# Kernel tuning notes

Hardware: AMD Instinct MI355X
Metric: run time of the kernel (lower is better)

## Reference

```python
import jax, jax.numpy as jnp
import numpy as np
from math import factorial

L_MAX = 3
K = 256
N = 2048


def _cg_coeff(l1, m1, l2, m2, l3, m3):
    # Clebsch-Gordan coefficient <l1 m1 l2 m2 | l3 m3> via the Racah formula.
    if m3 != m1 + m2:
        return 0.0
    pref = ((2 * l3 + 1) * factorial(l3 + l1 - l2) * factorial(l3 - l1 + l2)
            * factorial(l1 + l2 - l3) / factorial(l1 + l2 + l3 + 1)) ** 0.5
    pref *= (factorial(l3 + m3) * factorial(l3 - m3) * factorial(l1 - m1)
             * factorial(l1 + m1) * factorial(l2 - m2) * factorial(l2 + m2)) ** 0.5
    s = 0.0
    for k in range(0, l1 + l2 - l3 + 1):
        d = [k, l1 + l2 - l3 - k, l1 - m1 - k, l2 + m2 - k,
             l3 - l2 + m1 + k, l3 - l1 - m2 + k]
        if min(d) < 0:
            continue
        den = 1.0
        for x in d:
            den *= factorial(x)
        s += (-1.0) ** k / den
    return pref * s


def _cg_tensor(l1, l2, l3):
    out = np.zeros((2 * l1 + 1, 2 * l2 + 1, 2 * l3 + 1), dtype=np.float32)
    for m1 in range(-l1, l1 + 1):
        for m2 in range(-l2, l2 + 1):
            m3 = m1 + m2
            if -l3 <= m3 <= l3:
                out[m1 + l1, m2 + l2, m3 + l3] = _cg_coeff(l1, m1, l2, m2, l3, m3)
    return jnp.asarray(out)


# All (l1, l2) -> l coupling paths allowed by the triangle inequality, l <= L_MAX.
PATHS = {l: [(l1, l2) for l1 in range(L_MAX + 1) for l2 in range(L_MAX + 1)
             if abs(l1 - l2) <= l <= l1 + l2] for l in range(L_MAX + 1)}
CG = {(l1, l2, l): _cg_tensor(l1, l2, l)
      for l in range(L_MAX + 1) for (l1, l2) in PATHS[l]}


def _forward(f1, f2, U, W):
    outs = []
    for l in range(L_MAX + 1):
        # CG tensor product: elementwise over channels k, coupled over (m1, m2) -> m.
        parts = [jnp.einsum('abm,nak,nbk->nmk', CG[(l1, l2, l)], f1[l1], f2[l2])
                 for (l1, l2) in PATHS[l]]
        tp = jnp.concatenate(parts, axis=-1)          # [N, 2l+1, n_paths(l)*K]
        mixed = jnp.einsum('nmc,ck->nmk', tp, U[l])   # U_dict per-l mixing -> [N, 2l+1, K]
        mixed = jnp.einsum('nmk,kj->nmj', mixed, W[l])  # learned per-l linear
        outs.append(f1[l] + mixed)                    # residual
    return tuple(outs)


def setup_inputs() -> dict:
    key = jax.random.key(0)
    ks = jax.random.split(key, 16)
    inp = {}
    for l in range(L_MAX + 1):
        inp[f'f1_l{l}'] = jax.random.normal(ks[l], (N, 2 * l + 1, K), jnp.float32)
        inp[f'f2_l{l}'] = jax.random.normal(ks[4 + l], (N, 2 * l + 1, K), jnp.float32)
        cin = len(PATHS[l]) * K
        inp[f'U_{l}'] = jax.random.normal(ks[8 + l], (cin, K), jnp.float32) / float(np.sqrt(cin))
        inp[f'W_{l}'] = jax.random.normal(ks[12 + l], (K, K), jnp.float32) / float(np.sqrt(K))
    return inp


def reference(f1_l0, f1_l1, f1_l2, f1_l3,
              f2_l0, f2_l1, f2_l2, f2_l3,
              U_0, U_1, U_2, U_3,
              W_0, W_1, W_2, W_3):
    f1 = [f1_l0, f1_l1, f1_l2, f1_l3]
    f2 = [f2_l0, f2_l1, f2_l2, f2_l3]
    U = [U_0, U_1, U_2, U_3]
    W = [W_0, W_1, W_2, W_3]
    return _forward(f1, f2, U, W)
```

## Files before the change

kernel.cpp:

```cpp
#include <hip/hip_runtime.h>
#include <math.h>

typedef __attribute__((ext_vector_type(4))) float f32x4;
typedef __attribute__((ext_vector_type(8))) __bf16 bf16x8;
typedef __attribute__((ext_vector_type(4))) __bf16 bf16x4;

__device__ __constant__ int GP_L[34]  = {0,0,0,0, 1,1,1,1,1,1,1,1,1, 2,2,2,2,2,2,2,2,2,2,2, 3,3,3,3,3,3,3,3,3,3};
__device__ __constant__ int GP_L1[34] = {0,1,2,3, 0,1,1,1,2,2,2,3,3, 0,1,1,1,2,2,2,2,3,3,3, 0,1,1,2,2,2,3,3,3,3};
__device__ __constant__ int GP_L2[34] = {0,1,2,3, 1,0,1,2,1,2,3,2,3, 2,1,2,3,0,1,2,3,1,2,3, 3,2,3,1,2,3,0,1,2,3};

__device__ double dfact(int n) { double r = 1.0; for (int i = 2; i <= n; ++i) r *= (double)i; return r; }

__device__ double cg_coeff(int l1, int m1, int l2, int m2, int l3, int m3) {
  if (m3 != m1 + m2) return 0.0;
  double pref = sqrt((2.0 * l3 + 1.0) * dfact(l3 + l1 - l2) * dfact(l3 - l1 + l2)
                     * dfact(l1 + l2 - l3) / dfact(l1 + l2 + l3 + 1));
  pref *= sqrt(dfact(l3 + m3) * dfact(l3 - m3) * dfact(l1 - m1) * dfact(l1 + m1)
               * dfact(l2 - m2) * dfact(l2 + m2));
  double s = 0.0;
  for (int k = 0; k <= l1 + l2 - l3; ++k) {
    int d0 = k, d1 = l1 + l2 - l3 - k, d2 = l1 - m1 - k, d3 = l2 + m2 - k;
    int d4 = l3 - l2 + m1 + k, d5 = l3 - l1 - m2 + k;
    if (d0 < 0 || d1 < 0 || d2 < 0 || d3 < 0 || d4 < 0 || d5 < 0) continue;
    double den = dfact(d0) * dfact(d1) * dfact(d2) * dfact(d3) * dfact(d4) * dfact(d5);
    s += ((k & 1) ? -1.0 : 1.0) / den;
  }
  return pref * s;
}

__global__ void cg_init(float* __restrict__ cg) {
  int idx = blockIdx.x * 256 + threadIdx.x;
  if (idx >= 34 * 49) return;
  int gp = idx / 49, r = idx % 49;
  int m1i = r / 7, m2i = r % 7;
  int l3 = GP_L[gp], l1 = GP_L1[gp], l2 = GP_L2[gp];
  float v = 0.f;
  if (m1i <= 2 * l1 && m2i <= 2 * l2) {
    int m1 = m1i - l1, m2 = m2i - l2, m3 = m1 + m2;
    if (m3 >= -l3 && m3 <= l3) v = (float)cg_coeff(l1, m1, l2, m2, l3, m3);
  }
  cg[idx] = v;
}

__global__ __launch_bounds__(256) void cvt_u_all(
    const float* __restrict__ u0, const float* __restrict__ u1,
    const float* __restrict__ u2, const float* __restrict__ u3,
    __bf16* __restrict__ out) {
  long i = (long)blockIdx.x * 256 + threadIdx.x;
  const long b1 = 65536, b2 = 212992, b3 = 393216;
  const float* src; long s;
  if (i < b1)      { src = u0; s = i; }
  else if (i < b2) { src = u1; s = i - b1; }
  else if (i < b3) { src = u2; s = i - b2; }
  else             { src = u3; s = i - b3; }
  float4 v = ((const float4*)src)[s];
  bf16x4 o;
  o[0] = (__bf16)v.x; o[1] = (__bf16)v.y; o[2] = (__bf16)v.z; o[3] = (__bf16)v.w;
  ((bf16x4*)out)[i] = o;
}

__global__ void wt_cvt_all(const float* __restrict__ w0, const float* __restrict__ w1,
                           const float* __restrict__ w2, const float* __restrict__ w3,
                           __bf16* __restrict__ Wt) {
  int b = blockIdx.x;
  int l = b >> 8, j = b & 255, k = threadIdx.x;
  const float* W = (l == 0) ? w0 : (l == 1) ? w1 : (l == 2) ? w2 : w3;
  Wt[((long)l << 16) + (j << 8) + k] = (__bf16)W[(k << 8) + j];
}

template <int l1, int l2, int L>
__device__ __forceinline__ void tp_path2(const float* __restrict__ v1, const float* __restrict__ v2,
                                         const float* __restrict__ cgt, float* __restrict__ tp) {
#pragma unroll
  for (int a = 0; a < 2 * l1 + 1; ++a) {
#pragma unroll
    for (int b = 0; b < 2 * l2 + 1; ++b) {
      int mi = a + b - l1 - l2 + L;
      if (mi >= 0 && mi <= 2 * L)
        tp[mi] = fmaf(cgt[a * 7 + b], v1[a] * v2[b], tp[mi]);
    }
  }
}

#define TPW(LV, DST, CIN, GOFF, P, L1V, L2V)                                    \
  { float tp[2 * (LV) + 1] = {};                                                \
    tp_path2<L1V, L2V, LV>(v1 + CUM[L1V], v2 + CUM[L2V], cg + ((GOFF) + (P)) * 49, tp); \
    __bf16* o = (DST) + (n * (2 * (LV) + 1)) * (CIN) + (P) * 256 + k;           \
    _Pragma("unroll")                                                           \
    for (int m = 0; m < 2 * (LV) + 1; ++m) o[(long)m * (CIN)] = (__bf16)tp[m]; }

template <int LMASK>
__global__ __launch_bounds__(256) void tp_all(
    const float* __restrict__ f10, const float* __restrict__ f11,
    const float* __restrict__ f12, const float* __restrict__ f13,
    const float* __restrict__ f20, const float* __restrict__ f21,
    const float* __restrict__ f22, const float* __restrict__ f23,
    const float* __restrict__ cg,
    __bf16* __restrict__ A0, __bf16* __restrict__ A1,
    __bf16* __restrict__ A2, __bf16* __restrict__ A3) {
  const long n = blockIdx.x;
  const int k = threadIdx.x;
  constexpr int CUM[4] = {0, 1, 4, 9};
  const float* f1s[4] = {f10, f11, f12, f13};
  const float* f2s[4] = {f20, f21, f22, f23};

  float v1[16], v2[16];
#pragma unroll
  for (int l1 = 0; l1 < 4; ++l1) {
    const float* p1 = f1s[l1] + (n * (2 * l1 + 1)) * 256 + k;
    const float* p2 = f2s[l1] + (n * (2 * l1 + 1)) * 256 + k;
#pragma unroll
    for (int a = 0; a < 2 * l1 + 1; ++a) {
      v1[CUM[l1] + a] = p1[(long)a * 256];
      v2[CUM[l1] + a] = p2[(long)a * 256];
    }
  }

  if constexpr (LMASK & 1) {
    TPW(0, A0, 1024, 0, 0, 0, 0)  TPW(0, A0, 1024, 0, 1, 1, 1)
    TPW(0, A0, 1024, 0, 2, 2, 2)  TPW(0, A0, 1024, 0, 3, 3, 3)
  }
  if constexpr (LMASK & 2) {
    TPW(1, A1, 2304, 4, 0, 0, 1)  TPW(1, A1, 2304, 4, 1, 1, 0)
    TPW(1, A1, 2304, 4, 2, 1, 1)  TPW(1, A1, 2304, 4, 3, 1, 2)
    TPW(1, A1, 2304, 4, 4, 2, 1)  TPW(1, A1, 2304, 4, 5, 2, 2)
    TPW(1, A1, 2304, 4, 6, 2, 3)  TPW(1, A1, 2304, 4, 7, 3, 2)
    TPW(1, A1, 2304, 4, 8, 3, 3)
  }
  if constexpr (LMASK & 4) {
    TPW(2, A2, 2816, 13, 0, 0, 2)  TPW(2, A2, 2816, 13, 1, 1, 1)
    TPW(2, A2, 2816, 13, 2, 1, 2)  TPW(2, A2, 2816, 13, 3, 1, 3)
    TPW(2, A2, 2816, 13, 4, 2, 0)  TPW(2, A2, 2816, 13, 5, 2, 1)
    TPW(2, A2, 2816, 13, 6, 2, 2)  TPW(2, A2, 2816, 13, 7, 2, 3)
    TPW(2, A2, 2816, 13, 8, 3, 1)  TPW(2, A2, 2816, 13, 9, 3, 2)
    TPW(2, A2, 2816, 13, 10, 3, 3)
  }
  if constexpr (LMASK & 8) {
    TPW(3, A3, 2560, 24, 0, 0, 3)  TPW(3, A3, 2560, 24, 1, 1, 2)
    TPW(3, A3, 2560, 24, 2, 1, 3)  TPW(3, A3, 2560, 24, 3, 2, 1)
    TPW(3, A3, 2560, 24, 4, 2, 2)  TPW(3, A3, 2560, 24, 5, 2, 3)
    TPW(3, A3, 2560, 24, 6, 3, 0)  TPW(3, A3, 2560, 24, 7, 3, 1)
    TPW(3, A3, 2560, 24, 8, 3, 2)  TPW(3, A3, 2560, 24, 9, 3, 3)
  }
}

struct GemmDesc {
  const __bf16* A[4];
  const __bf16* B[4];
  void*         C[4];
  const float*  R[4];
  int start[4];
  int lmap[4];
  int Kd[4];
  int Nc[4];
};

__device__ __forceinline__ void gload_lds16(const void* g, void* l) {
  __builtin_amdgcn_global_load_lds((const __attribute__((address_space(1))) void*)g,
                                   (__attribute__((address_space(3))) void*)l, 16, 0, 0);
}

template <bool OUT_BF16, bool RESID>
__global__ __launch_bounds__(256) void gemm_batched(GemmDesc d) {
  __shared__ __bf16 As[128 * 64];
  __shared__ __bf16 Bs[128 * 64];
  const int tid = threadIdx.x;
  const int bid = blockIdx.x;
  int seg = 0;
  if (bid >= d.start[1]) seg = 1;
  if (bid >= d.start[2]) seg = 2;
  if (bid >= d.start[3]) seg = 3;
  const int l = d.lmap[seg];
  const int rel = bid - d.start[seg];
  const int Kd = d.Kd[l], Nc = d.Nc[l];
  const int nTN = Nc >> 7;
  const int tM = rel / nTN, tN = rel % nTN;

  const int lane = tid & 63, wave = tid >> 6;
  const int wm = (wave >> 1) << 6, wn = (wave & 1) << 6;
  const int lr = lane & 15, lk = (lane >> 4) << 3;

  f32x4 acc[4][4] = {};

  const int r32 = tid >> 3;
  const int sl = ((tid & 7) ^ (r32 & 7)) << 3;
  const __bf16* Ag = d.A[l] + (long)(tM * 128 + r32) * Kd + sl;
  const __bf16* Bg = d.B[l] + (long)(tN * 128 + r32) * Kd + sl;
  char* AsB = (char*)As;
  char* BsB = (char*)Bs;

  for (int kt = 0; kt < Kd; kt += 64) {
#pragma unroll
    for (int i = 0; i < 4; ++i) {
      gload_lds16(Ag + (long)i * 32 * Kd + kt, AsB + i * 4096 + tid * 16);
      gload_lds16(Bg + (long)i * 32 * Kd + kt, BsB + i * 4096 + tid * 16);
    }
    __syncthreads();

#pragma unroll
    for (int kk = 0; kk < 64; kk += 32) {
      bf16x8 af[4], bfr[4];
#pragma unroll
      for (int mi = 0; mi < 4; ++mi)
        af[mi] = *(const bf16x8*)(AsB + ((wm + mi * 16 + lr) << 7)
                                      + ((((kk + lk) << 1)) ^ ((lr & 7) << 4)));
#pragma unroll
      for (int ni = 0; ni < 4; ++ni)
        bfr[ni] = *(const bf16x8*)(BsB + ((wn + ni * 16 + lr) << 7)
                                       + ((((kk + lk) << 1)) ^ ((lr & 7) << 4)));
#pragma unroll
      for (int mi = 0; mi < 4; ++mi)
#pragma unroll
        for (int ni = 0; ni < 4; ++ni)
          acc[mi][ni] = __builtin_amdgcn_mfma_f32_16x16x32_bf16(af[mi], bfr[ni], acc[mi][ni], 0, 0, 0);
    }
    __syncthreads();
  }

  const long col0 = (long)tN * 128 + wn + lr;
  const long row0 = (long)tM * 128 + wm + ((lane >> 4) << 2);
#pragma unroll
  for (int mi = 0; mi < 4; ++mi) {
#pragma unroll
    for (int j = 0; j < 4; ++j) {
      long r = row0 + mi * 16 + j;
      long base = r * (long)Nc + col0;
#pragma unroll
      for (int ni = 0; ni < 4; ++ni) {
        long idx = base + ni * 16;
        float v = acc[mi][ni][j];
        if constexpr (RESID) v += d.R[l][idx];
        if constexpr (OUT_BF16) ((__bf16*)d.C[l])[idx] = (__bf16)v;
        else                    ((float*)d.C[l])[idx] = v;
      }
    }
  }
}

extern "C" void kernel_launch(void* const* d_in, const int* in_sizes, int n_in,
                              void* d_out, int out_size, void* d_ws, size_t ws_size,
                              hipStream_t stream) {
  const float* F1[4], * F2[4], * Uin[4], * Win[4];
  for (int l = 0; l < 4; ++l) {
    F1[l]  = (const float*)d_in[4 * l + 0];
    F2[l]  = (const float*)d_in[4 * l + 1];
    Uin[l] = (const float*)d_in[4 * l + 2];
    Win[l] = (const float*)d_in[4 * l + 3];
  }
  static const int  cin_[4]  = {1024, 2304, 2816, 2560};
  static const int  cum_[4]  = {0, 1024, 3328, 6144};
  static const long moff_[4] = {0, 524288, 2097152, 4718592};
  static const int  Ml_[4]   = {2048, 6144, 10240, 14336};
  static const long asz_[4]  = {4194304L, 28311552L, 57671680L, 73400320L};

  char* ws = (char*)d_ws;
  float*  cg   = (float*)ws;
  __bf16* Ubf  = (__bf16*)(ws + 8192);
  __bf16* Wtbf = (__bf16*)(ws + 8192 + 4456448);
  __bf16* UWt  = (__bf16*)(ws + 5242880);
  const long ABASE = 10485760;
  const bool big = ws_size >= (size_t)(ABASE + asz_[0] + asz_[1] + asz_[2] + asz_[3]);

  __bf16* Ab[4];
  if (big) {
    long off = ABASE;
    for (int l = 0; l < 4; ++l) { Ab[l] = (__bf16*)(ws + off); off += asz_[l]; }
  } else {
    for (int l = 0; l < 4; ++l) Ab[l] = (__bf16*)(ws + ABASE);
  }

  hipLaunchKernelGGL(cg_init, dim3(7), dim3(256), 0, stream, cg);
  hipLaunchKernelGGL(cvt_u_all, dim3(2176), dim3(256), 0, stream,
                     Uin[0], Uin[1], Uin[2], Uin[3], Ubf);
  hipLaunchKernelGGL(wt_cvt_all, dim3(1024), dim3(256), 0, stream,
                     Win[0], Win[1], Win[2], Win[3], Wtbf);

  {
    GemmDesc d;
    int starts[4] = {0, 40, 84, 120};
    int lmap[4]   = {3, 2, 1, 0};
    for (int s = 0; s < 4; ++s) { d.start[s] = starts[s]; d.lmap[s] = lmap[s]; }
    for (int l = 0; l < 4; ++l) {
      d.A[l] = Wtbf + (long)l * 65536;
      d.B[l] = Ubf + (long)cum_[l] * 256;
      d.C[l] = (void*)(UWt + (long)cum_[l] * 256);
      d.R[l] = nullptr;
      d.Kd[l] = 256;
      d.Nc[l] = cin_[l];
    }
    hipLaunchKernelGGL((gemm_batched<true, false>), dim3(136), dim3(256), 0, stream, d);
  }

  if (big) {
    hipLaunchKernelGGL((tp_all<15>), dim3(2048), dim3(256), 0, stream,
                       F1[0], F1[1], F1[2], F1[3], F2[0], F2[1], F2[2], F2[3],
                       cg, Ab[0], Ab[1], Ab[2], Ab[3]);
    GemmDesc d;
    int starts[4] = {0, 224, 384, 480};
    int lmap[4]   = {3, 2, 1, 0};
    for (int s = 0; s < 4; ++s) { d.start[s] = starts[s]; d.lmap[s] = lmap[s]; }
    for (int l = 0; l < 4; ++l) {
      d.A[l] = Ab[l];
      d.B[l] = UWt + (long)cum_[l] * 256;
      d.C[l] = (void*)((float*)d_out + moff_[l]);
      d.R[l] = F1[l];
      d.Kd[l] = cin_[l];
      d.Nc[l] = 256;
    }
    hipLaunchKernelGGL((gemm_batched<false, true>), dim3(512), dim3(256), 0, stream, d);
  } else {
    for (int l = 0; l < 4; ++l) {
      switch (l) {
        case 0: hipLaunchKernelGGL((tp_all<1>), dim3(2048), dim3(256), 0, stream,
                  F1[0],F1[1],F1[2],F1[3], F2[0],F2[1],F2[2],F2[3], cg,
                  Ab[0],Ab[1],Ab[2],Ab[3]); break;
        case 1: hipLaunchKernelGGL((tp_all<2>), dim3(2048), dim3(256), 0, stream,
                  F1[0],F1[1],F1[2],F1[3], F2[0],F2[1],F2[2],F2[3], cg,
                  Ab[0],Ab[1],Ab[2],Ab[3]); break;
        case 2: hipLaunchKernelGGL((tp_all<4>), dim3(2048), dim3(256), 0, stream,
                  F1[0],F1[1],F1[2],F1[3], F2[0],F2[1],F2[2],F2[3], cg,
                  Ab[0],Ab[1],Ab[2],Ab[3]); break;
        case 3: hipLaunchKernelGGL((tp_all<8>), dim3(2048), dim3(256), 0, stream,
                  F1[0],F1[1],F1[2],F1[3], F2[0],F2[1],F2[2],F2[3], cg,
                  Ab[0],Ab[1],Ab[2],Ab[3]); break;
      }
      GemmDesc d;
      for (int s = 0; s < 4; ++s) {
        d.start[s] = (s == 0) ? 0 : 0x7fffffff;
        d.lmap[s] = l;
      }
      for (int ll = 0; ll < 4; ++ll) {
        d.A[ll] = Ab[l];
        d.B[ll] = UWt + (long)cum_[l] * 256;
        d.C[ll] = (void*)((float*)d_out + moff_[l]);
        d.R[ll] = F1[l];
        d.Kd[ll] = cin_[l];
        d.Nc[ll] = 256;
      }
      hipLaunchKernelGGL((gemm_batched<false, true>), dim3((Ml_[l] >> 7) * 2), dim3(256),
                         0, stream, d);
    }
  }
  (void)in_sizes; (void)n_in; (void)out_size; (void)ws_size;
}
```

Baseline: 152.6 us.

## Fuse tensor product generation into GEMM, computing A tiles directly in LDS

Replaces the separate tensor-product kernel and the big GEMM with one fused kernel. Each K-tile of the A operand (the CG products) is computed on the fly into swizzled LDS while the UW weight tile streams in via global_load_lds, and MFMA accumulation follows with the residual added at the end. This removes the write and re-read of the large bf16 intermediate A buffers (up to roughly 160MB) and one launch. In exchange, f1/f2 rows are re-read for every path, MFMA row tiles are small (48-64 rows) with some padding, and the TP math is serialised with the MMA under two barriers per K-step.

Result: slower. 186.8 us (+22.4%).

```diff
diff --git a/kernel.cpp b/kernel.cpp
--- a/kernel.cpp
+++ b/kernel.cpp
@@ -2,8 +2,10 @@
 #include <math.h>
 
 typedef __attribute__((ext_vector_type(4))) float f32x4;
+typedef __attribute__((ext_vector_type(2))) float f32x2;
 typedef __attribute__((ext_vector_type(8))) __bf16 bf16x8;
 typedef __attribute__((ext_vector_type(4))) __bf16 bf16x4;
+typedef __attribute__((ext_vector_type(2))) __bf16 bf16x2;
 
 __device__ __constant__ int GP_L[34]  = {0,0,0,0, 1,1,1,1,1,1,1,1,1, 2,2,2,2,2,2,2,2,2,2,2, 3,3,3,3,3,3,3,3,3,3};
 __device__ __constant__ int GP_L1[34] = {0,1,2,3, 0,1,1,1,2,2,2,3,3, 0,1,1,1,2,2,2,2,3,3,3, 0,1,1,2,2,2,3,3,3,3};
@@ -68,82 +70,6 @@
   Wt[((long)l << 16) + (j << 8) + k] = (__bf16)W[(k << 8) + j];
 }
 
-template <int l1, int l2, int L>
-__device__ __forceinline__ void tp_path2(const float* __restrict__ v1, const float* __restrict__ v2,
-                                         const float* __restrict__ cgt, float* __restrict__ tp) {
-#pragma unroll
-  for (int a = 0; a < 2 * l1 + 1; ++a) {
-#pragma unroll
-    for (int b = 0; b < 2 * l2 + 1; ++b) {
-      int mi = a + b - l1 - l2 + L;
-      if (mi >= 0 && mi <= 2 * L)
-        tp[mi] = fmaf(cgt[a * 7 + b], v1[a] * v2[b], tp[mi]);
-    }
-  }
-}
-
-#define TPW(LV, DST, CIN, GOFF, P, L1V, L2V)                                    \
-  { float tp[2 * (LV) + 1] = {};                                                \
-    tp_path2<L1V, L2V, LV>(v1 + CUM[L1V], v2 + CUM[L2V], cg + ((GOFF) + (P)) * 49, tp); \
-    __bf16* o = (DST) + (n * (2 * (LV) + 1)) * (CIN) + (P) * 256 + k;           \
-    _Pragma("unroll")                                                           \
-    for (int m = 0; m < 2 * (LV) + 1; ++m) o[(long)m * (CIN)] = (__bf16)tp[m]; }
-
-template <int LMASK>
-__global__ __launch_bounds__(256) void tp_all(
-    const float* __restrict__ f10, const float* __restrict__ f11,
-    const float* __restrict__ f12, const float* __restrict__ f13,
-    const float* __restrict__ f20, const float* __restrict__ f21,
-    const float* __restrict__ f22, const float* __restrict__ f23,
-    const float* __restrict__ cg,
-    __bf16* __restrict__ A0, __bf16* __restrict__ A1,
-    __bf16* __restrict__ A2, __bf16* __restrict__ A3) {
-  const long n = blockIdx.x;
-  const int k = threadIdx.x;
-  constexpr int CUM[4] = {0, 1, 4, 9};
-  const float* f1s[4] = {f10, f11, f12, f13};
-  const float* f2s[4] = {f20, f21, f22, f23};
-
-  float v1[16], v2[16];
-#pragma unroll
-  for (int l1 = 0; l1 < 4; ++l1) {
-    const float* p1 = f1s[l1] + (n * (2 * l1 + 1)) * 256 + k;
-    const float* p2 = f2s[l1] + (n * (2 * l1 + 1)) * 256 + k;
-#pragma unroll
-    for (int a = 0; a < 2 * l1 + 1; ++a) {
-      v1[CUM[l1] + a] = p1[(long)a * 256];
-      v2[CUM[l1] + a] = p2[(long)a * 256];
-    }
-  }
-
-  if constexpr (LMASK & 1) {
-    TPW(0, A0, 1024, 0, 0, 0, 0)  TPW(0, A0, 1024, 0, 1, 1, 1)
-    TPW(0, A0, 1024, 0, 2, 2, 2)  TPW(0, A0, 1024, 0, 3, 3, 3)
-  }
-  if constexpr (LMASK & 2) {
-    TPW(1, A1, 2304, 4, 0, 0, 1)  TPW(1, A1, 2304, 4, 1, 1, 0)
-    TPW(1, A1, 2304, 4, 2, 1, 1)  TPW(1, A1, 2304, 4, 3, 1, 2)
-    TPW(1, A1, 2304, 4, 4, 2, 1)  TPW(1, A1, 2304, 4, 5, 2, 2)
-    TPW(1, A1, 2304, 4, 6, 2, 3)  TPW(1, A1, 2304, 4, 7, 3, 2)
-    TPW(1, A1, 2304, 4, 8, 3, 3)
-  }
-  if constexpr (LMASK & 4) {
-    TPW(2, A2, 2816, 13, 0, 0, 2)  TPW(2, A2, 2816, 13, 1, 1, 1)
-    TPW(2, A2, 2816, 13, 2, 1, 2)  TPW(2, A2, 2816, 13, 3, 1, 3)
-    TPW(2, A2, 2816, 13, 4, 2, 0)  TPW(2, A2, 2816, 13, 5, 2, 1)
-    TPW(2, A2, 2816, 13, 6, 2, 2)  TPW(2, A2, 2816, 13, 7, 2, 3)
-    TPW(2, A2, 2816, 13, 8, 3, 1)  TPW(2, A2, 2816, 13, 9, 3, 2)
-    TPW(2, A2, 2816, 13, 10, 3, 3)
-  }
-  if constexpr (LMASK & 8) {
-    TPW(3, A3, 2560, 24, 0, 0, 3)  TPW(3, A3, 2560, 24, 1, 1, 2)
-    TPW(3, A3, 2560, 24, 2, 1, 3)  TPW(3, A3, 2560, 24, 3, 2, 1)
-    TPW(3, A3, 2560, 24, 4, 2, 2)  TPW(3, A3, 2560, 24, 5, 2, 3)
-    TPW(3, A3, 2560, 24, 6, 3, 0)  TPW(3, A3, 2560, 24, 7, 3, 1)
-    TPW(3, A3, 2560, 24, 8, 3, 2)  TPW(3, A3, 2560, 24, 9, 3, 3)
-  }
-}
-
 struct GemmDesc {
   const __bf16* A[4];
   const __bf16* B[4];
@@ -237,6 +163,164 @@
   }
 }
 
+struct FusedArgs {
+  const float* f1[4];
+  const float* f2[4];
+  const float* cg;
+  const __bf16* UWt;
+  float* out;
+};
+
+template <int L, int L1V, int L2V>
+__device__ __forceinline__ void tp_pass(
+    const float* __restrict__ f1, const float* __restrict__ f2,
+    long n, int kc, int k2, const float* __restrict__ cgt,
+    char* __restrict__ AsB, int row0) {
+  f32x2 v1[2 * L1V + 1], v2[2 * L2V + 1];
+  const float* p1 = f1 + (n * (2 * L1V + 1)) * 256 + kc + k2;
+  const float* p2 = f2 + (n * (2 * L2V + 1)) * 256 + kc + k2;
+#pragma unroll
+  for (int a = 0; a < 2 * L1V + 1; ++a) v1[a] = *(const f32x2*)(p1 + a * 256);
+#pragma unroll
+  for (int b = 0; b < 2 * L2V + 1; ++b) v2[b] = *(const f32x2*)(p2 + b * 256);
+  f32x2 tp[2 * L + 1];
+#pragma unroll
+  for (int m = 0; m < 2 * L + 1; ++m) { tp[m][0] = 0.f; tp[m][1] = 0.f; }
+#pragma unroll
+  for (int a = 0; a < 2 * L1V + 1; ++a)
+#pragma unroll
+    for (int b = 0; b < 2 * L2V + 1; ++b) {
+      const int m = a + b - (L1V + L2V - L);
+      if (m >= 0 && m <= 2 * L) {
+        float c = cgt[a * 7 + b];
+        tp[m][0] = fmaf(c, v1[a][0] * v2[b][0], tp[m][0]);
+        tp[m][1] = fmaf(c, v1[a][1] * v2[b][1], tp[m][1]);
+      }
+    }
+#pragma unroll
+  for (int m = 0; m < 2 * L + 1; ++m) {
+    int row = row0 + m;
+    int byte = row * 128 + ((k2 << 1) ^ ((row & 7) << 4));
+    bf16x2 o; o[0] = (__bf16)tp[m][0]; o[1] = (__bf16)tp[m][1];
+    *(bf16x2*)(AsB + byte) = o;
+  }
+}
+
+#define TPC(P, AA, BB)                                                          \
+  case P: {                                                                     \
+    _Pragma("unroll")                                                           \
+    for (int ps = 0; ps < NPASS; ++ps)                                          \
+      tp_pass<L, AA, BB>(Af.f1[AA], Af.f2[BB], n0 + ps * 8 + nloc, kc, k2,      \
+                         cgb + (GOFF + P) * 49, AsB, (ps * 8 + nloc) * (2 * L + 1)); \
+  } break;
+
+template <int L>
+__device__ __forceinline__ void fused_seg(
+    const FusedArgs& Af, int rel, char* __restrict__ AsB, char* __restrict__ BsB,
+    const __bf16* __restrict__ Bmat, float* __restrict__ Cout,
+    const float* __restrict__ Resid, int cin) {
+  constexpr int NB    = (L == 0) ? 64 : (L == 1) ? 16 : 8;
+  constexpr int TROWS = (L == 0 || L == 3) ? 64 : 48;
+  constexpr int VALID = NB * (2 * L + 1);
+  constexpr int MR    = TROWS / 16;
+  constexpr int NPASS = NB / 8;
+  constexpr int GOFF  = (L == 0) ? 0 : (L == 1) ? 4 : (L == 2) ? 13 : 24;
+
+  const int tid = threadIdx.x;
+  const int lane = tid & 63, wave = tid >> 6;
+  const long n0 = (long)rel * NB;
+  const int nloc = tid >> 5;
+  const int k2 = (tid & 31) << 1;
+  const float* cgb = Af.cg;
+
+  if constexpr (VALID < TROWS) {
+    if (tid < (TROWS - VALID) * 8) {
+      f32x4 z = {0.f, 0.f, 0.f, 0.f};
+      *(f32x4*)(AsB + (VALID + (tid >> 3)) * 128 + (tid & 7) * 16) = z;
+    }
+  }
+
+  f32x4 acc[MR][4];
+#pragma unroll
+  for (int i = 0; i < MR; ++i)
+#pragma unroll
+    for (int j = 0; j < 4; ++j) acc[i][j] = {0.f, 0.f, 0.f, 0.f};
+
+  const __bf16* Bg = Bmat + (long)(tid >> 3) * cin + (((tid & 7) ^ ((tid >> 3) & 7)) << 3);
+
+  for (int kt = 0; kt < cin; kt += 64) {
+#pragma unroll
+    for (int i = 0; i < 8; ++i)
+      gload_lds16(Bg + (long)i * 32 * cin + kt, BsB + i * 4096 + tid * 16);
+
+    const int p = kt >> 8, kc = kt & 255;
+    if constexpr (L == 0) {
+      switch (p) { TPC(0,0,0) TPC(1,1,1) TPC(2,2,2) TPC(3,3,3) default: break; }
+    } else if constexpr (L == 1) {
+      switch (p) { TPC(0,0,1) TPC(1,1,0) TPC(2,1,1) TPC(3,1,2) TPC(4,2,1)
+                   TPC(5,2,2) TPC(6,2,3) TPC(7,3,2) TPC(8,3,3) default: break; }
+    } else if constexpr (L == 2) {
+      switch (p) { TPC(0,0,2) TPC(1,1,1) TPC(2,1,2) TPC(3,1,3) TPC(4,2,0)
+                   TPC(5,2,1) TPC(6,2,2) TPC(7,2,3) TPC(8,3,1) TPC(9,3,2)
+                   TPC(10,3,3) default: break; }
+    } else {
+      switch (p) { TPC(0,0,3) TPC(1,1,2) TPC(2,1,3) TPC(3,2,1) TPC(4,2,2)
+                   TPC(5,2,3) TPC(6,3,0) TPC(7,3,1) TPC(8,3,2) TPC(9,3,3)
+                   default: break; }
+    }
+
+    __syncthreads();
+
+#pragma unroll
+    for (int kk = 0; kk < 64; kk += 32) {
+      const int kb = ((kk + ((lane >> 4) << 3)) << 1) ^ ((lane & 7) << 4);
+      bf16x8 af[MR], bfr[4];
+#pragma unroll
+      for (int mi = 0; mi < MR; ++mi)
+        af[mi] = *(const bf16x8*)(AsB + (mi * 16 + (lane & 15)) * 128 + kb);
+#pragma unroll
+      for (int ni = 0; ni < 4; ++ni)
+        bfr[ni] = *(const bf16x8*)(BsB + ((wave << 6) + ni * 16 + (lane & 15)) * 128 + kb);
+#pragma unroll
+      for (int mi = 0; mi < MR; ++mi)
+#pragma unroll
+        for (int ni = 0; ni < 4; ++ni)
+          acc[mi][ni] = __builtin_amdgcn_mfma_f32_16x16x32_bf16(af[mi], bfr[ni], acc[mi][ni], 0, 0, 0);
+    }
+    __syncthreads();
+  }
+
+  const int col = (wave << 6) + (lane & 15);
+  const int rb = (lane >> 4) << 2;
+#pragma unroll
+  for (int mi = 0; mi < MR; ++mi)
+#pragma unroll
+    for (int j = 0; j < 4; ++j) {
+      int r = mi * 16 + rb + j;
+      if (VALID < TROWS && r >= VALID) continue;
+      long idx = ((long)rel * VALID + r) * 256 + col;
+#pragma unroll
+      for (int ni = 0; ni < 4; ++ni)
+        Cout[idx + ni * 16] = acc[mi][ni][j] + Resid[idx + ni * 16];
+    }
+}
+
+__global__ __launch_bounds__(256, 2) void fused_kernel(FusedArgs Af) {
+  __shared__ __align__(16) char sm[8192 + 32768];
+  char* AsB = sm;
+  char* BsB = sm + 8192;
+  const int bid = blockIdx.x;
+  if (bid < 256) {
+    fused_seg<2>(Af, bid, AsB, BsB, Af.UWt + 3328L * 256, Af.out + 2097152L, Af.f1[2], 2816);
+  } else if (bid < 512) {
+    fused_seg<3>(Af, bid - 256, AsB, BsB, Af.UWt + 6144L * 256, Af.out + 4718592L, Af.f1[3], 2560);
+  } else if (bid < 640) {
+    fused_seg<1>(Af, bid - 512, AsB, BsB, Af.UWt + 1024L * 256, Af.out + 524288L, Af.f1[1], 2304);
+  } else {
+    fused_seg<0>(Af, bid - 640, AsB, BsB, Af.UWt, Af.out, Af.f1[0], 1024);
+  }
+}
+
 extern "C" void kernel_launch(void* const* d_in, const int* in_sizes, int n_in,
                               void* d_out, int out_size, void* d_ws, size_t ws_size,
                               hipStream_t stream) {
@@ -247,27 +331,14 @@
     Uin[l] = (const float*)d_in[4 * l + 2];
     Win[l] = (const float*)d_in[4 * l + 3];
   }
-  static const int  cin_[4]  = {1024, 2304, 2816, 2560};
-  static const int  cum_[4]  = {0, 1024, 3328, 6144};
-  static const long moff_[4] = {0, 524288, 2097152, 4718592};
-  static const int  Ml_[4]   = {2048, 6144, 10240, 14336};
-  static const long asz_[4]  = {4194304L, 28311552L, 57671680L, 73400320L};
+  static const int cin_[4] = {1024, 2304, 2816, 2560};
+  static const int cum_[4] = {0, 1024, 3328, 6144};
 
   char* ws = (char*)d_ws;
   float*  cg   = (float*)ws;
   __bf16* Ubf  = (__bf16*)(ws + 8192);
   __bf16* Wtbf = (__bf16*)(ws + 8192 + 4456448);
   __bf16* UWt  = (__bf16*)(ws + 5242880);
-  const long ABASE = 10485760;
-  const bool big = ws_size >= (size_t)(ABASE + asz_[0] + asz_[1] + asz_[2] + asz_[3]);
-
-  __bf16* Ab[4];
-  if (big) {
-    long off = ABASE;
-    for (int l = 0; l < 4; ++l) { Ab[l] = (__bf16*)(ws + off); off += asz_[l]; }
-  } else {
-    for (int l = 0; l < 4; ++l) Ab[l] = (__bf16*)(ws + ABASE);
-  }
 
   hipLaunchKernelGGL(cg_init, dim3(7), dim3(256), 0, stream, cg);
   hipLaunchKernelGGL(cvt_u_all, dim3(2176), dim3(256), 0, stream,
@@ -291,55 +362,13 @@
     hipLaunchKernelGGL((gemm_batched<true, false>), dim3(136), dim3(256), 0, stream, d);
   }
 
-  if (big) {
-    hipLaunchKernelGGL((tp_all<15>), dim3(2048), dim3(256), 0, stream,
-                       F1[0], F1[1], F1[2], F1[3], F2[0], F2[1], F2[2], F2[3],
-                       cg, Ab[0], Ab[1], Ab[2], Ab[3]);
-    GemmDesc d;
-    int starts[4] = {0, 224, 384, 480};
-    int lmap[4]   = {3, 2, 1, 0};
-    for (int s = 0; s < 4; ++s) { d.start[s] = starts[s]; d.lmap[s] = lmap[s]; }
-    for (int l = 0; l < 4; ++l) {
-      d.A[l] = Ab[l];
-      d.B[l] = UWt + (long)cum_[l] * 256;
-      d.C[l] = (void*)((float*)d_out + moff_[l]);
-      d.R[l] = F1[l];
-      d.Kd[l] = cin_[l];
-      d.Nc[l] = 256;
-    }
-    hipLaunchKernelGGL((gemm_batched<false, true>), dim3(512), dim3(256), 0, stream, d);
-  } else {
-    for (int l = 0; l < 4; ++l) {
-      switch (l) {
-        case 0: hipLaunchKernelGGL((tp_all<1>), dim3(2048), dim3(256), 0, stream,
-                  F1[0],F1[1],F1[2],F1[3], F2[0],F2[1],F2[2],F2[3], cg,
-                  Ab[0],Ab[1],Ab[2],Ab[3]); break;
-        case 1: hipLaunchKernelGGL((tp_all<2>), dim3(2048), dim3(256), 0, stream,
-                  F1[0],F1[1],F1[2],F1[3], F2[0],F2[1],F2[2],F2[3], cg,
-                  Ab[0],Ab[1],Ab[2],Ab[3]); break;
-        case 2: hipLaunchKernelGGL((tp_all<4>), dim3(2048), dim3(256), 0, stream,
-                  F1[0],F1[1],F1[2],F1[3], F2[0],F2[1],F2[2],F2[3], cg,
-                  Ab[0],Ab[1],Ab[2],Ab[3]); break;
-        case 3: hipLaunchKernelGGL((tp_all<8>), dim3(2048), dim3(256), 0, stream,
-                  F1[0],F1[1],F1[2],F1[3], F2[0],F2[1],F2[2],F2[3], cg,
-                  Ab[0],Ab[1],Ab[2],Ab[3]); break;
-      }
-      GemmDesc d;
-      for (int s = 0; s < 4; ++s) {
-        d.start[s] = (s == 0) ? 0 : 0x7fffffff;
-        d.lmap[s] = l;
-      }
-      for (int ll = 0; ll < 4; ++ll) {
-        d.A[ll] = Ab[l];
-        d.B[ll] = UWt + (long)cum_[l] * 256;
-        d.C[ll] = (void*)((float*)d_out + moff_[l]);
-        d.R[ll] = F1[l];
-        d.Kd[ll] = cin_[l];
-        d.Nc[ll] = 256;
-      }
-      hipLaunchKernelGGL((gemm_batched<false, true>), dim3((Ml_[l] >> 7) * 2), dim3(256),
-                         0, stream, d);
-    }
+  {
+    FusedArgs a;
+    for (int l = 0; l < 4; ++l) { a.f1[l] = F1[l]; a.f2[l] = F2[l]; }
+    a.cg = cg;
+    a.UWt = UWt;
+    a.out = (float*)d_out;
+    hipLaunchKernelGGL(fused_kernel, dim3(672), dim3(256), 0, stream, a);
   }
   (void)in_sizes; (void)n_in; (void)out_size; (void)ws_size;
 }
```
